# Performance work log

Measured on AMD Instinct MI355X. Metric: run time of the kernel, lower is better.

Reference implementation:

```python
import jax, jax.numpy as jnp
import numpy as np

DIM = 2048
HIDDEN = 2048
HEADS = 4
HD = HIDDEN // HEADS  # head_dim = 512
EPS = 1e-6
BATCH = 4
SEQ = 2048


def setup_inputs() -> dict:
    key = jax.random.key(0)
    k0, k1, k2, k3 = jax.random.split(key, 4)
    s = 0.02  # typical init scale; keeps exp() input gate well-behaved
    x = jax.random.normal(k0, (BATCH, SEQ, DIM), dtype=jnp.float32)
    W_in = (jax.random.normal(k1, (HIDDEN, DIM), dtype=jnp.float32) * s)
    W_gate = (jax.random.normal(k2, (4 * HIDDEN, HIDDEN), dtype=jnp.float32) * s)
    b_gate = jnp.zeros((4 * HIDDEN,), dtype=jnp.float32)
    rms_w = jnp.ones((HD,), dtype=jnp.float32)
    W_out = (jax.random.normal(k3, (DIM, HIDDEN), dtype=jnp.float32) * s)
    return {"x": x, "W_in": W_in, "W_gate": W_gate, "b_gate": b_gate,
            "rms_w": rms_w, "W_out": W_out}


def reference(x, W_in, W_gate, b_gate, rms_w, W_out):
    B, L, _ = x.shape
    # in_proj then gate_proj (the rearrange round-trip in torch is an identity
    # on the flat hidden dim, so gates come straight from x @ W_in.T)
    xp = x @ W_in.T                                    # (B, L, HIDDEN)
    gates = xp @ W_gate.T + b_gate                     # (B, L, 4*HIDDEN)
    # rearrange 'b l (h d) -> b h l d' with h=HEADS, d=4*HD
    gates = gates.reshape(B, L, HEADS, 4 * HD).transpose(0, 2, 1, 3)
    i_g, f_g, o_g, c_t = jnp.split(gates, 4, axis=-1)  # each (B, H, L, HD)
    i_g = jnp.exp(i_g)            # exponential input gate
    f_g = jax.nn.sigmoid(f_g)
    o_g = jax.nn.sigmoid(o_g)
    c_t = jnp.tanh(c_t)

    # time-major for the recurrent scan: (L, B, H, HD)
    tm = lambda a: jnp.moveaxis(a, 2, 0)

    def step(c, g):
        i, f, o, cd = g
        c = f * c + i * cd                                         # cell update
        c_norm = c * jax.lax.rsqrt(jnp.mean(c * c, axis=-1, keepdims=True) + EPS) * rms_w
        h = o * jnp.tanh(c_norm)
        return c, h

    c0 = jnp.zeros((B, HEADS, HD), dtype=x.dtype)
    _, hs = jax.lax.scan(step, c0, (tm(i_g), tm(f_g), tm(o_g), tm(c_t)))
    # (L, B, H, HD) -> (B, L, H*HD)
    h_out = jnp.moveaxis(hs, 0, 1).reshape(B, L, HIDDEN)
    return h_out @ W_out.T                             # (B, L, DIM)
```

## Files before the change

kernel.cpp:

```cpp
#include <hip/hip_runtime.h>
#include <hip/hip_bf16.h>
#include <stdint.h>

#define DIMN    2048
#define HIDDEN  2048
#define NHEADS  4
#define HDIM    512
#define BATCH   4
#define SEQ     2048
#define NTOK    (BATCH*SEQ)
#define G4      (4*HIDDEN)
#define EPSV    1e-6f
#define CHUNK   128
#define NCHUNK  (SEQ/CHUNK)

typedef short short8 __attribute__((ext_vector_type(8)));
typedef float floatx4 __attribute__((ext_vector_type(4)));

union BV8 { uint4 u; __hip_bfloat16 h[8]; unsigned short s[8]; };

__device__ __forceinline__ float fast_sigmoid(float x) {
    return 1.0f / (1.0f + __expf(-x));
}
__device__ __forceinline__ float fast_tanh(float x) {
    return 1.0f - 2.0f / (__expf(2.0f * x) + 1.0f);
}
__device__ __forceinline__ float b2f(unsigned short u) {
    union { unsigned int ui; float f; } v; v.ui = ((unsigned int)u) << 16; return v.f;
}

__device__ __forceinline__ void gld_lds16(const void* gp, void* lp) {
    __builtin_amdgcn_global_load_lds(
        (const __attribute__((address_space(1))) void*)gp,
        (__attribute__((address_space(3))) void*)lp, 16, 0, 0);
}

__global__ __launch_bounds__(256) void cast_f32_bf16(
    const float* __restrict__ in, __hip_bfloat16* __restrict__ out, int n8)
{
    int i = blockIdx.x * 256 + threadIdx.x;
    if (i >= n8) return;
    const float4* p = (const float4*)(in + (size_t)i * 8);
    float4 a = p[0], b = p[1];
    BV8 v;
    v.h[0] = __float2bfloat16(a.x); v.h[1] = __float2bfloat16(a.y);
    v.h[2] = __float2bfloat16(a.z); v.h[3] = __float2bfloat16(a.w);
    v.h[4] = __float2bfloat16(b.x); v.h[5] = __float2bfloat16(b.y);
    v.h[6] = __float2bfloat16(b.z); v.h[7] = __float2bfloat16(b.w);
    *(uint4*)(out + (size_t)i * 8) = v.u;
}

template <int EPILOGUE, int ASRC>
__global__ __launch_bounds__(256, 1) void gemm256(
    const __hip_bfloat16* __restrict__ A,
    const __hip_bfloat16* __restrict__ Bt,
    void* __restrict__ Cout,
    const float* __restrict__ bias,
    int M, int N, int K, int lda)
{
    __shared__ __align__(16) short sA[2][256 * 64];
    __shared__ __align__(16) short sB[2][256 * 64];

    const int tid  = threadIdx.x;
    const int wave = tid >> 6, lane = tid & 63;
    const int wm = wave >> 1, wn = wave & 1;
    const int quad = lane >> 4, lr = lane & 15;
    const int r8  = lane >> 3;
    const int gcs = ((lane & 7) ^ r8) * 8;
    const int rl7 = lr & 7;

    const int gx   = gridDim.x;
    const int nwg  = gx * gridDim.y;
    const int orig = blockIdx.y * gx + blockIdx.x;
    const int wg   = (orig & 7) * (nwg >> 3) + (orig >> 3);
    const int bm = wg / gx, bn = wg % gx;

    const short* Ag = (const short*)A + (size_t)(bm * 256) * lda;
    const short* Bg = (const short*)Bt + (size_t)(bn * 256) * K;

    floatx4 acc[8][8];
#pragma unroll
    for (int i = 0; i < 8; ++i)
#pragma unroll
        for (int j = 0; j < 8; ++j) acc[i][j] = (floatx4)0.0f;

    const int NT = K >> 6;

    auto stageAB = [&](int kt) {
        const int kb = kt << 6;
        size_t acol;
        if (ASRC == 0) acol = (size_t)(kb + gcs);
        else           acol = (size_t)(((kb >> 9) << 11) + (kb & 511) + gcs);
        short* dA = &sA[kt & 1][0];
        short* dB = &sB[kt & 1][0];
#pragma unroll
        for (int c = 0; c < 8; ++c) {
            const int base = c * 32 + wave * 8;
            const int grow = base + r8;
            gld_lds16(Ag + (size_t)grow * lda + acol,   dA + base * 64);
            gld_lds16(Bg + (size_t)grow * K + kb + gcs, dB + base * 64);
        }
    };

    stageAB(0);
    asm volatile("s_waitcnt vmcnt(0)" ::: "memory");
    __builtin_amdgcn_s_barrier();

    short8 av[8], bv[8];

    for (int t = 0; t < NT; ++t) {
        const short* lA = &sA[t & 1][0];
        const short* lB = &sB[t & 1][0];

        {
            const int co = ((quad ^ rl7) << 3);
#pragma unroll
            for (int mt = 0; mt < 8; ++mt)
                av[mt] = *(const short8*)&lA[(wm * 128 + mt * 16 + lr) * 64 + co];
#pragma unroll
            for (int nt = 0; nt < 8; ++nt)
                bv[nt] = *(const short8*)&lB[(wn * 128 + nt * 16 + lr) * 64 + co];
        }
        if (t + 1 < NT) stageAB(t + 1);
#pragma unroll
        for (int mt = 0; mt < 8; ++mt)
#pragma unroll
            for (int nt = 0; nt < 8; ++nt)
                acc[mt][nt] = __builtin_amdgcn_mfma_f32_16x16x32_bf16(
                    av[mt], bv[nt], acc[mt][nt], 0, 0, 0);

        {
            const int co = (((4 + quad) ^ rl7) << 3);
#pragma unroll
            for (int mt = 0; mt < 8; ++mt)
                av[mt] = *(const short8*)&lA[(wm * 128 + mt * 16 + lr) * 64 + co];
#pragma unroll
            for (int nt = 0; nt < 8; ++nt)
                bv[nt] = *(const short8*)&lB[(wn * 128 + nt * 16 + lr) * 64 + co];
        }
#pragma unroll
        for (int mt = 0; mt < 8; ++mt)
#pragma unroll
            for (int nt = 0; nt < 8; ++nt)
                acc[mt][nt] = __builtin_amdgcn_mfma_f32_16x16x32_bf16(
                    av[mt], bv[nt], acc[mt][nt], 0, 0, 0);

        if (t + 1 < NT) asm volatile("s_waitcnt vmcnt(0)" ::: "memory");
        __builtin_amdgcn_s_barrier();
    }

    const int colbase = bn * 256 + wn * 128;
    const int rowbase = bm * 256 + wm * 128;

    if (EPILOGUE == 0) {
        __hip_bfloat16* O = (__hip_bfloat16*)Cout;
#pragma unroll
        for (int mt = 0; mt < 8; ++mt)
#pragma unroll
            for (int nt = 0; nt < 8; ++nt)
#pragma unroll
                for (int r = 0; r < 4; ++r) {
                    int row = rowbase + mt * 16 + quad * 4 + r;
                    int col = colbase + nt * 16 + lr;
                    O[(size_t)row * N + col] = __float2bfloat16(acc[mt][nt][r]);
                }
    } else if (EPILOGUE == 1) {
        __hip_bfloat16* O = (__hip_bfloat16*)Cout;
#pragma unroll
        for (int nt = 0; nt < 8; ++nt) {
            int col = colbase + nt * 16 + lr;
            int g = (col >> 9) & 3;
            float bvs = bias[col];
#pragma unroll
            for (int mt = 0; mt < 8; ++mt)
#pragma unroll
                for (int r = 0; r < 4; ++r) {
                    int row = rowbase + mt * 16 + quad * 4 + r;
                    float v = acc[mt][nt][r] + bvs;
                    if (g == 0)       v = __expf(v);
                    else if (g == 3)  v = fast_tanh(v);
                    else              v = fast_sigmoid(v);
                    O[(size_t)row * N + col] = __float2bfloat16(v);
                }
        }
    } else {
        float* O = (float*)Cout;
#pragma unroll
        for (int mt = 0; mt < 8; ++mt)
#pragma unroll
            for (int nt = 0; nt < 8; ++nt)
#pragma unroll
                for (int r = 0; r < 4; ++r) {
                    int row = rowbase + mt * 16 + quad * 4 + r;
                    int col = colbase + nt * 16 + lr;
                    O[(size_t)row * N + col] = acc[mt][nt][r];
                }
    }
}

struct G16 { unsigned short i[16], f[16], c[16]; };

__device__ __forceinline__ void load_g16(const unsigned short* __restrict__ g,
                                         int t0, G16& o)
{
#pragma unroll
    for (int j = 0; j < 16; ++j) {
        const unsigned short* gp = g + (size_t)(t0 + j) * G4;
        o.i[j] = gp[0]; o.f[j] = gp[512]; o.c[j] = gp[1536];
    }
}
__device__ __forceinline__ void comp_sum16(const G16& gg, float& c, float& P)
{
#pragma unroll
    for (int j = 0; j < 16; ++j) {
        float iv = b2f(gg.i[j]);
        float fv = b2f(gg.f[j]);
        float cd = b2f(gg.c[j]);
        c = fmaf(fv, c, iv * cd);
        P *= fv;
    }
}
__device__ __forceinline__ float comp_lds16(const G16& gg, float c,
                                            __hip_bfloat16* __restrict__ sc,
                                            int t0, int d)
{
#pragma unroll
    for (int j = 0; j < 16; ++j) {
        float iv = b2f(gg.i[j]);
        float fv = b2f(gg.f[j]);
        float cd = b2f(gg.c[j]);
        c = fmaf(fv, c, iv * cd);
        sc[(t0 + j) * HDIM + d] = __float2bfloat16(c);
    }
    return c;
}

__global__ __launch_bounds__(256) void scan_pass1(
    const __hip_bfloat16* __restrict__ gates,
    float* __restrict__ cLast, float* __restrict__ PLast)
{
    int blk = blockIdx.x;
    int dh = blk & 1;
    int j  = (blk >> 1) & 15;
    int bh = blk >> 5;
    int b = bh >> 2, h = bh & 3;
    int d = dh * 256 + threadIdx.x;
    int bhd = bh * 512 + d;

    const unsigned short* g = (const unsigned short*)gates
        + (size_t)(b * SEQ + j * CHUNK) * G4 + h * 2048 + d;

    float c = 0.0f, P = 1.0f;
    G16 A, B;
    load_g16(g, 0, A);
    for (int t0 = 0; t0 < CHUNK; t0 += 32) {
        load_g16(g, t0 + 16, B);
        comp_sum16(A, c, P);
        if (t0 + 32 < CHUNK) load_g16(g, t0 + 32, A);
        comp_sum16(B, c, P);
    }
    cLast[j * 8192 + bhd] = c;
    PLast[j * 8192 + bhd] = P;
}

__global__ __launch_bounds__(512) void scan_pass2_norm(
    const __hip_bfloat16* __restrict__ gates_c,
    const float* __restrict__ cLast, const float* __restrict__ PLast,
    __hip_bfloat16* __restrict__ gates,
    const float* __restrict__ rms_w)
{
    __shared__ __hip_bfloat16 sc[CHUNK * HDIM];

    int blk = blockIdx.x;
    int j  = blk & 15;
    int bh = blk >> 4;
    int b = bh >> 2, h = bh & 3;
    int d = threadIdx.x;
    int bhd = bh * 512 + d;

    float c = 0.0f;
    for (int k = 0; k < j; ++k)
        c = fmaf(PLast[k * 8192 + bhd], c, cLast[k * 8192 + bhd]);

    const unsigned short* g = (const unsigned short*)gates_c
        + (size_t)(b * SEQ + j * CHUNK) * G4 + h * 2048 + d;

    G16 A, B;
    load_g16(g, 0, A);
    for (int t0 = 0; t0 < CHUNK; t0 += 32) {
        load_g16(g, t0 + 16, B);
        c = comp_lds16(A, c, sc, t0, d);
        if (t0 + 32 < CHUNK) load_g16(g, t0 + 32, A);
        c = comp_lds16(B, c, sc, t0 + 16, d);
    }
    __syncthreads();

    const int wave = threadIdx.x >> 6, lane = threadIdx.x & 63;

    float4 w0 = *(const float4*)&rms_w[lane * 8];
    float4 w1 = *(const float4*)&rms_w[lane * 8 + 4];
    float w[8] = { w0.x, w0.y, w0.z, w0.w, w1.x, w1.y, w1.z, w1.w };

    for (int it = 0; it < 16; ++it) {
        int t = wave * 16 + it;
        size_t tok = (size_t)(b * SEQ + j * CHUNK + t);

        BV8 cv; cv.u = *(const uint4*)&sc[t * HDIM + lane * 8];
        float cf[8]; float s = 0.0f;
#pragma unroll
        for (int q = 0; q < 8; ++q) { cf[q] = b2f(cv.s[q]); s += cf[q] * cf[q]; }
#pragma unroll
        for (int off = 32; off > 0; off >>= 1) s += __shfl_xor(s, off, 64);
        float rs = rsqrtf(s * (1.0f / 512.0f) + EPSV);

        BV8 ov; ov.u = *(const uint4*)(gates + tok * G4 + h * 2048 + 1024 + lane * 8);
        BV8 hv;
#pragma unroll
        for (int q = 0; q < 8; ++q) {
            float o = b2f(ov.s[q]);
            hv.h[q] = __float2bfloat16(o * fast_tanh(cf[q] * rs * w[q]));
        }
        *(uint4*)(gates + tok * G4 + h * 2048 + lane * 8) = hv.u;
    }
}

extern "C" void kernel_launch(void* const* d_in, const int* in_sizes, int n_in,
                              void* d_out, int out_size, void* d_ws, size_t ws_size,
                              hipStream_t stream)
{
    const float* x      = (const float*)d_in[0];
    const float* W_in   = (const float*)d_in[1];
    const float* W_gate = (const float*)d_in[2];
    const float* b_gate = (const float*)d_in[3];
    const float* rms_w  = (const float*)d_in[4];
    const float* W_out  = (const float*)d_in[5];
    float* out = (float*)d_out;

    char* base = (char*)d_ws;
    __hip_bfloat16* wgb   = (__hip_bfloat16*)base;
    __hip_bfloat16* xpb   = (__hip_bfloat16*)(base + (((size_t)32) << 20));
    __hip_bfloat16* gates = (__hip_bfloat16*)(base + (((size_t)64) << 20));
    __hip_bfloat16* wib  = gates;
    __hip_bfloat16* xb   = (__hip_bfloat16*)(base + (((size_t)72) << 20));
    __hip_bfloat16* wob  = wgb;
    float* cLast = (float*)(base + (((size_t)8) << 20));
    float* PLast = (float*)(base + (((size_t)8) << 20) + (512 << 10));

    cast_f32_bf16<<<(HIDDEN * DIMN) / 8 / 256, 256, 0, stream>>>(W_in, wib, (HIDDEN * DIMN) / 8);
    cast_f32_bf16<<<(NTOK * DIMN) / 8 / 256, 256, 0, stream>>>(x, xb, (NTOK * DIMN) / 8);
    cast_f32_bf16<<<(G4 * HIDDEN) / 8 / 256, 256, 0, stream>>>(W_gate, wgb, (G4 * HIDDEN) / 8);

    {
        dim3 grid(HIDDEN / 256, NTOK / 256);
        gemm256<0, 0><<<grid, 256, 0, stream>>>(xb, wib, xpb, nullptr,
                                                NTOK, HIDDEN, DIMN, DIMN);
    }
    {
        dim3 grid(G4 / 256, NTOK / 256);
        gemm256<1, 0><<<grid, 256, 0, stream>>>(xpb, wgb, gates, b_gate,
                                                NTOK, G4, HIDDEN, HIDDEN);
    }
    cast_f32_bf16<<<(DIMN * HIDDEN) / 8 / 256, 256, 0, stream>>>(W_out, wob, (DIMN * HIDDEN) / 8);

    scan_pass1<<<BATCH * NHEADS * NCHUNK * 2, 256, 0, stream>>>(gates, cLast, PLast);
    scan_pass2_norm<<<BATCH * NHEADS * NCHUNK, 512, 0, stream>>>(gates, cLast, PLast,
                                                                 gates, rms_w);

    {
        dim3 grid(DIMN / 256, NTOK / 256);
        gemm256<2, 1><<<grid, 256, 0, stream>>>(gates, wob, out, nullptr,
                                                NTOK, DIMN, HIDDEN, G4);
    }
}
```

Measured before the change: 750.2 us.

## Split GEMM tile across eight waves and raise MFMA issue priority

Doubles the GEMM workgroup from 256 to 512 threads (8 waves, 2x4 arrangement), so each wave computes a 128x64 sub-tile. That halves the accumulator and B-fragment register footprint per wave. Global-to-LDS staging is rewritten into separate A and B passes with permuted row placement that matches the new wave-to-fragment mapping. The next-tile prefetch now starts before the LDS fragment reads, and the MFMA blocks are wrapped in s_setprio. The aim is better latency hiding through more waves, at the cost of more LDS reads per MFMA, since each B fragment is now shared by fewer MFMAs.

```diff
diff --git a/kernel.cpp b/kernel.cpp
--- a/kernel.cpp
+++ b/kernel.cpp
@@ -51,7 +51,7 @@
 }
 
 template <int EPILOGUE, int ASRC>
-__global__ __launch_bounds__(256, 1) void gemm256(
+__global__ __launch_bounds__(512, 2) void gemm256(
     const __hip_bfloat16* __restrict__ A,
     const __hip_bfloat16* __restrict__ Bt,
     void* __restrict__ Cout,
@@ -63,7 +63,7 @@
 
     const int tid  = threadIdx.x;
     const int wave = tid >> 6, lane = tid & 63;
-    const int wm = wave >> 1, wn = wave & 1;
+    const int wm = wave >> 2, wn = wave & 3;
     const int quad = lane >> 4, lr = lane & 15;
     const int r8  = lane >> 3;
     const int gcs = ((lane & 7) ^ r8) * 8;
@@ -78,78 +78,100 @@
     const short* Ag = (const short*)A + (size_t)(bm * 256) * lda;
     const short* Bg = (const short*)Bt + (size_t)(bn * 256) * K;
 
-    floatx4 acc[8][8];
+    floatx4 acc[8][4];
 #pragma unroll
     for (int i = 0; i < 8; ++i)
 #pragma unroll
-        for (int j = 0; j < 8; ++j) acc[i][j] = (floatx4)0.0f;
+        for (int j = 0; j < 4; ++j) acc[i][j] = (floatx4)0.0f;
 
     const int NT = K >> 6;
 
-    auto stageAB = [&](int kt) {
+    auto stageA = [&](int kt, int qm) {
         const int kb = kt << 6;
         size_t acol;
         if (ASRC == 0) acol = (size_t)(kb + gcs);
         else           acol = (size_t)(((kb >> 9) << 11) + (kb & 511) + gcs);
-        short* dA = &sA[kt & 1][0];
-        short* dB = &sB[kt & 1][0];
-#pragma unroll
-        for (int c = 0; c < 8; ++c) {
-            const int base = c * 32 + wave * 8;
-            const int grow = base + r8;
-            gld_lds16(Ag + (size_t)grow * lda + acol,   dA + base * 64);
-            gld_lds16(Bg + (size_t)grow * K + kb + gcs, dB + base * 64);
+        short* dst = &sA[kt & 1][0];
+#pragma unroll
+        for (int e = 0; e < 2; ++e) {
+            const int base = qm * 128 + e * 64 + wave * 8;
+            const int row  = base + r8;
+            const int grow = ((row >> 6) & 1) * 128 + qm * 64 + (row & 63);
+            gld_lds16(Ag + (size_t)grow * lda + acol, dst + base * 64);
         }
     };
-
-    stageAB(0);
+    auto stageB = [&](int kt, int qn) {
+        const int kb = kt << 6;
+        short* dst = &sB[kt & 1][0];
+#pragma unroll
+        for (int e = 0; e < 2; ++e) {
+            const int base = qn * 128 + e * 64 + wave * 8;
+            const int row  = base + r8;
+            const int grow = ((row >> 5) & 3) * 64 + qn * 32 + (row & 31);
+            gld_lds16(Bg + (size_t)grow * K + kb + gcs, dst + base * 64);
+        }
+    };
+    auto stageAll = [&](int kt) {
+        stageA(kt, 0); stageA(kt, 1); stageB(kt, 0); stageB(kt, 1);
+    };
+
+    stageAll(0);
     asm volatile("s_waitcnt vmcnt(0)" ::: "memory");
     __builtin_amdgcn_s_barrier();
 
-    short8 av[8], bv[8];
+    short8 av[8], bv[4];
 
     for (int t = 0; t < NT; ++t) {
         const short* lA = &sA[t & 1][0];
         const short* lB = &sB[t & 1][0];
 
+        if (t + 1 < NT) stageAll(t + 1);
+
         {
             const int co = ((quad ^ rl7) << 3);
 #pragma unroll
             for (int mt = 0; mt < 8; ++mt)
-                av[mt] = *(const short8*)&lA[(wm * 128 + mt * 16 + lr) * 64 + co];
-#pragma unroll
-            for (int nt = 0; nt < 8; ++nt)
-                bv[nt] = *(const short8*)&lB[(wn * 128 + nt * 16 + lr) * 64 + co];
-        }
-        if (t + 1 < NT) stageAB(t + 1);
+                av[mt] = *(const short8*)&lA[
+                    ((mt >= 4 ? 128 : 0) + wm * 64 + (mt & 3) * 16 + lr) * 64 + co];
+#pragma unroll
+            for (int nt = 0; nt < 4; ++nt)
+                bv[nt] = *(const short8*)&lB[
+                    ((nt >= 2 ? 128 : 0) + wn * 32 + (nt & 1) * 16 + lr) * 64 + co];
+        }
+        __builtin_amdgcn_s_setprio(1);
 #pragma unroll
         for (int mt = 0; mt < 8; ++mt)
 #pragma unroll
-            for (int nt = 0; nt < 8; ++nt)
+            for (int nt = 0; nt < 4; ++nt)
                 acc[mt][nt] = __builtin_amdgcn_mfma_f32_16x16x32_bf16(
                     av[mt], bv[nt], acc[mt][nt], 0, 0, 0);
+        __builtin_amdgcn_s_setprio(0);
 
         {
             const int co = (((4 + quad) ^ rl7) << 3);
 #pragma unroll
             for (int mt = 0; mt < 8; ++mt)
-                av[mt] = *(const short8*)&lA[(wm * 128 + mt * 16 + lr) * 64 + co];
-#pragma unroll
-            for (int nt = 0; nt < 8; ++nt)
-                bv[nt] = *(const short8*)&lB[(wn * 128 + nt * 16 + lr) * 64 + co];
-        }
+                av[mt] = *(const short8*)&lA[
+                    ((mt >= 4 ? 128 : 0) + wm * 64 + (mt & 3) * 16 + lr) * 64 + co];
+#pragma unroll
+            for (int nt = 0; nt < 4; ++nt)
+                bv[nt] = *(const short8*)&lB[
+                    ((nt >= 2 ? 128 : 0) + wn * 32 + (nt & 1) * 16 + lr) * 64 + co];
+        }
+        __builtin_amdgcn_s_setprio(1);
 #pragma unroll
         for (int mt = 0; mt < 8; ++mt)
 #pragma unroll
-            for (int nt = 0; nt < 8; ++nt)
+            for (int nt = 0; nt < 4; ++nt)
                 acc[mt][nt] = __builtin_amdgcn_mfma_f32_16x16x32_bf16(
                     av[mt], bv[nt], acc[mt][nt], 0, 0, 0);
+        __builtin_amdgcn_s_setprio(0);
 
         if (t + 1 < NT) asm volatile("s_waitcnt vmcnt(0)" ::: "memory");
         __builtin_amdgcn_s_barrier();
     }
 
-    const int colbase = bn * 256 + wn * 128;
+    const int colbase = bn * 256 + wn * 64;
     const int rowbase = bm * 256 + wm * 128;
 
     if (EPILOGUE == 0) {
@@ -157,7 +179,7 @@
 #pragma unroll
         for (int mt = 0; mt < 8; ++mt)
 #pragma unroll
-            for (int nt = 0; nt < 8; ++nt)
+            for (int nt = 0; nt < 4; ++nt)
 #pragma unroll
                 for (int r = 0; r < 4; ++r) {
                     int row = rowbase + mt * 16 + quad * 4 + r;
@@ -167,7 +189,7 @@
     } else if (EPILOGUE == 1) {
         __hip_bfloat16* O = (__hip_bfloat16*)Cout;
 #pragma unroll
-        for (int nt = 0; nt < 8; ++nt) {
+        for (int nt = 0; nt < 4; ++nt) {
             int col = colbase + nt * 16 + lr;
             int g = (col >> 9) & 3;
             float bvs = bias[col];
@@ -188,7 +210,7 @@
 #pragma unroll
         for (int mt = 0; mt < 8; ++mt)
 #pragma unroll
-            for (int nt = 0; nt < 8; ++nt)
+            for (int nt = 0; nt < 4; ++nt)
 #pragma unroll
                 for (int r = 0; r < 4; ++r) {
                     int row = rowbase + mt * 16 + quad * 4 + r;
@@ -352,12 +374,12 @@
 
     {
         dim3 grid(HIDDEN / 256, NTOK / 256);
-        gemm256<0, 0><<<grid, 256, 0, stream>>>(xb, wib, xpb, nullptr,
+        gemm256<0, 0><<<grid, 512, 0, stream>>>(xb, wib, xpb, nullptr,
                                                 NTOK, HIDDEN, DIMN, DIMN);
     }
     {
         dim3 grid(G4 / 256, NTOK / 256);
-        gemm256<1, 0><<<grid, 256, 0, stream>>>(xpb, wgb, gates, b_gate,
+        gemm256<1, 0><<<grid, 512, 0, stream>>>(xpb, wgb, gates, b_gate,
                                                 NTOK, G4, HIDDEN, HIDDEN);
     }
     cast_f32_bf16<<<(DIMN * HIDDEN) / 8 / 256, 256, 0, stream>>>(W_out, wob, (DIMN * HIDDEN) / 8);
@@ -368,7 +390,7 @@
 
     {
         dim3 grid(DIMN / 256, NTOK / 256);
-        gemm256<2, 1><<<grid, 256, 0, stream>>>(gates, wob, out, nullptr,
+        gemm256<2, 1><<<grid, 512, 0, stream>>>(gates, wob, out, nullptr,
                                                 NTOK, DIMN, HIDDEN, G4);
     }
 }
```

New measurement: 685.1 us. 8.7% less time.
